# Kernel tuning notes

Hardware: AMD Instinct MI355X
Metric: run time of the kernel (lower is better)

## Reference

```python
import jax, jax.numpy as jnp
import numpy as np

N_E = 16384
E_DIM = 64
BETA = 0.25


def setup_inputs() -> dict:
    key = jax.random.key(0)
    k1, k2 = jax.random.split(key)
    z = jax.random.normal(k1, (8, E_DIM, 32, 32), dtype=jnp.float32)
    # original inits uniform(-1/n_e, 1/n_e); use same scale
    emb_w = jax.random.uniform(k2, (N_E, E_DIM), dtype=jnp.float32,
                               minval=-1.0 / N_E, maxval=1.0 / N_E)
    return {"z": z, "emb_w": emb_w}


def reference(z, emb_w):
    # b c h w -> b h w c
    zp = jnp.transpose(z, (0, 2, 3, 1))              # [B,H,W,C]
    zf = zp.reshape(-1, E_DIM)                       # [N, e_dim]

    # pairwise squared distances: ||z||^2 + ||e||^2 - 2 z e^T
    d = (jnp.sum(zf * zf, axis=1, keepdims=True)
         + jnp.sum(emb_w * emb_w, axis=1)
         - 2.0 * jnp.einsum('nd,kd->nk', zf, emb_w))  # [N, n_e]
    idx = jnp.argmin(d, axis=1)                      # [N] int

    # usage tracking (codebook_usage starts at zeros each fresh module)
    usage = jnp.zeros((N_E,), dtype=jnp.float32).at[idx].max(1.0)
    num_unique = jnp.sum(usage).astype(jnp.int32)
    total_usage = jnp.sum(usage) / N_E

    z_q = emb_w[idx].reshape(zp.shape)               # [B,H,W,C]

    # legacy loss: ||sg(z_q)-z||^2 + beta*||z_q-sg(z)||^2
    loss = (jnp.mean((jax.lax.stop_gradient(z_q) - zp) ** 2)
            + BETA * jnp.mean((z_q - jax.lax.stop_gradient(zp)) ** 2))

    # straight-through estimator
    z_q = zp + jax.lax.stop_gradient(z_q - zp)
    z_q = jnp.transpose(z_q, (0, 3, 1, 2))           # b h w c -> b c h w

    return (z_q, loss, idx, num_unique, usage, total_usage)
```

## Files before the change

### kernel.cpp

```cpp
#include <hip/hip_runtime.h>
#include <math.h>

#define N_ROWS 8192
#define N_E    16384
#define EDIM   64
#define KSPLIT 16
#define KPER   1024
#define CHUNK  64
#define NCH    (KPER/CHUNK)

#define OFF_ZQ    0
#define OFF_LOSS  524288
#define OFF_IDX   524289
#define OFF_NUNIQ 532481
#define OFF_USAGE 532482
#define OFF_TOTAL 548866

typedef __attribute__((ext_vector_type(8)))  short  short8;
typedef __attribute__((ext_vector_type(8)))  ushort ushort8;
typedef __attribute__((ext_vector_type(4)))  float  f32x4;

__device__ ushort g_eh[N_E * EDIM];
__device__ ushort g_zh[N_ROWS * EDIM];
__device__ float  g_zt[N_ROWS * EDIM];

__device__ __forceinline__ ushort bf16hi(float v) {
    unsigned u = __float_as_uint(v);
    return (ushort)((u + 0x7fffu + ((u >> 16) & 1u)) >> 16);
}

__global__ __launch_bounds__(256) void vq_split(
    const float* __restrict__ z, const float* __restrict__ emb,
    float* __restrict__ anorm, float* __restrict__ out,
    float* __restrict__ lossacc, unsigned* __restrict__ done)
{
    __shared__ float lds[64][129];
    int bid = blockIdx.x, t = threadIdx.x;
    if (bid < 1024) {
        int i = bid * 256 + t;
        float4 v = ((const float4*)emb)[i];
        ushort4 h;
        h.x = bf16hi(v.x); h.y = bf16hi(v.y);
        h.z = bf16hi(v.z); h.w = bf16hi(v.w);
        ((ushort4*)g_eh)[i] = h;
    } else if (bid < 1088) {
        int zb = bid - 1024;
        int b = zb >> 3, hw0 = (zb & 7) << 7;
        const float* zp = z + (size_t)b * 65536 + hw0;
        for (int i = 0; i < 32; i++) {
            int j = i * 256 + t;
            int d = j >> 7, hw = j & 127;
            lds[d][hw] = zp[d * 1024 + hw];
        }
        __syncthreads();
        for (int i = 0; i < 4; i++) {
            int task = i * 256 + t;
            int hw = task >> 3, oct = task & 7;
            ushort8 h8; float4 f0, f1;
            float* fp0 = (float*)&f0; float* fp1 = (float*)&f1;
#pragma unroll
            for (int q = 0; q < 8; q++) {
                float v = lds[oct * 8 + q][hw];
                ((ushort*)&h8)[q] = bf16hi(v);
                if (q < 4) fp0[q] = v; else fp1[q - 4] = v;
            }
            size_t ro = (size_t)(b * 1024 + hw0 + hw) * 64 + oct * 8;
            *(ushort8*)(g_zh + ro) = h8;
            *(float4*)(g_zt + ro) = f0;
            *(float4*)(g_zt + ro + 4) = f1;
        }
        if (t < 128) {
            double s = 0.0;
            for (int d = 0; d < 64; d++) {
                float v = lds[d][t];
                s += (double)(v * v);
            }
            anorm[b * 1024 + hw0 + t] = (float)s;
        }
    } else {
        int i = (bid - 1088) * 256 + t;
        out[OFF_USAGE + i] = 0.f;
        if (bid == 1088 && t == 0) { *lossacc = 0.f; *done = 0u; }
    }
}

__global__ __launch_bounds__(256) void vq_mfma(const float* __restrict__ anorm,
                                               unsigned* __restrict__ pcand)
{
    __shared__ __align__(16) ushort ebuf[2][8][CHUNK][8];

    const int t = threadIdx.x;
    const int w = t >> 6, lane = t & 63;
    const int rb = blockIdx.x >> 4, split = blockIdx.x & 15;
    const int n0 = rb * 128;
    const int nw = n0 + w * 32;
    const int kbase = split * KPER;
    const int col = lane & 15, quad = lane >> 4;

    short8 ah[2][2];
#pragma unroll
    for (int rt = 0; rt < 2; rt++)
#pragma unroll
        for (int s = 0; s < 2; s++) {
            size_t off = (size_t)(nw + rt * 16 + col) * 64 + s * 32 + quad * 8;
            ah[rt][s] = *(const short8*)(g_zh + off);
        }

    float av[8];
#pragma unroll
    for (int rt = 0; rt < 2; rt++)
#pragma unroll
        for (int r = 0; r < 4; r++)
            av[rt * 4 + r] = anorm[nw + rt * 16 + quad * 4 + r];

    unsigned p1[8], p2[8];
#pragma unroll
    for (int s = 0; s < 8; s++) { p1[s] = 0xFFFFFFFFu; p2[s] = 0xFFFFFFFFu; }

    auto stage = [&](int dbuf, int code0) {
#pragma unroll
        for (int jj = 0; jj < 2; jj++) {
            int g = w * 2 + jj;
            const ushort* ga = g_eh + (size_t)(code0 + lane) * 64 + g * 8;
            __builtin_amdgcn_global_load_lds(
                (const __attribute__((address_space(1))) void*)ga,
                (__attribute__((address_space(3))) void*)&ebuf[dbuf][g][0][0],
                16, 0, 0);
        }
    };

    const f32x4 Z = {0.f, 0.f, 0.f, 0.f};
    stage(0, kbase);
    for (int ch = 0; ch < NCH; ch++) {
        int cur = ch & 1;
        if (ch + 1 < NCH) {
            stage(cur ^ 1, kbase + (ch + 1) * CHUNK);
            asm volatile("s_waitcnt vmcnt(2)" ::: "memory");
        } else {
            asm volatile("s_waitcnt vmcnt(0)" ::: "memory");
        }
        __builtin_amdgcn_s_barrier();
        asm volatile("" ::: "memory");
#pragma unroll
        for (int ct = 0; ct < 4; ct++) {
            int cn = ct * 16 + col;
            short8 bh0 = *(const short8*)&ebuf[cur][quad][cn][0];
            short8 bh1 = *(const short8*)&ebuf[cur][4 + quad][cn][0];
            f32x4 a0 = __builtin_amdgcn_mfma_f32_16x16x32_bf16(ah[0][0], bh0, Z, 0, 0, 0);
            f32x4 a1 = __builtin_amdgcn_mfma_f32_16x16x32_bf16(ah[1][0], bh0, Z, 0, 0, 0);
            a0 = __builtin_amdgcn_mfma_f32_16x16x32_bf16(ah[0][1], bh1, a0, 0, 0, 0);
            a1 = __builtin_amdgcn_mfma_f32_16x16x32_bf16(ah[1][1], bh1, a1, 0, 0, 0);

            unsigned slot = (unsigned)(ch * 4 + ct);
#pragma unroll
            for (int rt = 0; rt < 2; rt++)
#pragma unroll
                for (int r = 0; r < 4; r++) {
                    int s = rt * 4 + r;
                    float c = rt ? a1[r] : a0[r];
                    float dq = fmaf(-2.0f, c, av[s]);
                    unsigned e = (__float_as_uint(dq) << 6) | slot;
                    unsigned p2n;
                    asm("v_med3_u32 %0, %1, %2, %3"
                        : "=v"(p2n) : "v"(p1[s]), "v"(p2[s]), "v"(e));
                    p2[s] = p2n;
                    p1[s] = (p1[s] < e) ? p1[s] : e;
                }
        }
        __builtin_amdgcn_s_barrier();
        asm volatile("" ::: "memory");
    }

    unsigned* sc = (unsigned*)ebuf;
#pragma unroll
    for (int s = 0; s < 8; s++) {
        int rt = s >> 2, r = s & 3;
        int lr = w * 32 + rt * 16 + quad * 4 + r;
        unsigned av26 = __float_as_uint(av[s]) & 0x03FFFFFFu;
#pragma unroll
        for (int j = 0; j < 2; j++) {
            unsigned p = j ? p2[s] : p1[s];
            unsigned dq26 = p >> 6;
            int diff = ((int)((dq26 - av26) << 6)) >> 6;
            unsigned packed = ((unsigned)(diff + 32768) << 10)
                            | ((p & 63u) << 4) | (unsigned)col;
            sc[lr * 32 + ((col * 2 + j + lr * 2) & 31)] = packed;
        }
    }
    __syncthreads();
    if (t < 128) {
        unsigned b0 = ~0u, b1 = ~0u, b2 = ~0u, b3 = ~0u;
        for (int q = 0; q < 32; q++) {
            unsigned v = sc[t * 32 + ((q + 2 * t) & 31)];
            unsigned m0 = (b0 > v) ? b0 : v;  b0 = (b0 < v) ? b0 : v;
            unsigned m1 = (b1 > m0) ? b1 : m0; b1 = (b1 < m0) ? b1 : m0;
            unsigned m2 = (b2 > m1) ? b2 : m1; b2 = (b2 < m1) ? b2 : m1;
            b3 = (b3 < m2) ? b3 : m2;
        }
        size_t base = (size_t)(n0 + t) * (KSPLIT * 4) + split * 4;
        pcand[base + 0] = b0; pcand[base + 1] = b1;
        pcand[base + 2] = b2; pcand[base + 3] = b3;
    }
}

__device__ __forceinline__ double shfl_xor_d(double p, int m) {
    int2 u = __builtin_bit_cast(int2, p);
    u.x = __shfl_xor(u.x, m);
    u.y = __shfl_xor(u.y, m);
    return __builtin_bit_cast(double, u);
}
__device__ __forceinline__ unsigned long long shfl_xor_u64(unsigned long long p, int m) {
    int2 u = __builtin_bit_cast(int2, p);
    u.x = __shfl_xor(u.x, m);
    u.y = __shfl_xor(u.y, m);
    return __builtin_bit_cast(unsigned long long, u);
}

__global__ __launch_bounds__(256) void vq_refine(
    const float* __restrict__ emb, const float* __restrict__ anorm,
    const unsigned* __restrict__ pcand,
    float* __restrict__ out, int* __restrict__ idxfin)
{
    int t = threadIdx.x;
    int lane = t & 63;
    int n = blockIdx.x * 4 + (t >> 6);
    int li = lane & 15;
    int qd = lane >> 4;

    float4 zf = *(const float4*)(g_zt + (size_t)n * 64 + li * 4);
    double z0 = (double)zf.x, z1 = (double)zf.y;
    double z2 = (double)zf.z, z3 = (double)zf.w;

    float av = anorm[n];
    unsigned av_b = __float_as_uint(av);

    unsigned v = pcand[(size_t)n * 64 + lane];
    unsigned dqb = av_b + (v >> 10) - 32768u;
    float cd = __uint_as_float(dqb);
    int ck = (lane >> 2) * KPER + (int)((v >> 4) & 63u) * 16 + (int)(v & 15u);

    float mn = cd;
#pragma unroll
    for (int s = 1; s < 64; s <<= 1) mn = fminf(mn, __shfl_xor(mn, s));
    float margin = __uint_as_float(av_b & 0xFF800000u) * 0x1p-18f;
    unsigned long long msk = __ballot(cd <= mn + margin);

    unsigned long long bkey = ~0ull;
    while (msk) {
        int ls[4];
#pragma unroll
        for (int j = 0; j < 4; j++) {
            ls[j] = msk ? (__ffsll((unsigned long long)msk) - 1) : -1;
            if (msk) msk &= msk - 1;
        }
        int lsel = ls[qd];
        int lsafe = (lsel >= 0) ? lsel : 0;
        int kq = __shfl(ck, lsafe);
        int k = (lsel >= 0) ? kq : -1;
        double s = 0.0;
        if (k >= 0) {
            float4 ef = *(const float4*)(emb + (size_t)k * EDIM + li * 4);
            s = fma(z3, (double)ef.w,
                fma(z2, (double)ef.z,
                fma(z1, (double)ef.y, z0 * (double)ef.x)));
        }
        s += shfl_xor_d(s, 1);
        s += shfl_xor_d(s, 2);
        s += shfl_xor_d(s, 4);
        s += shfl_xor_d(s, 8);
        if (k >= 0) {
            float c32 = (float)s;
            float dq = av - 2.0f * c32;
            unsigned long long key =
                ((unsigned long long)__float_as_uint(dq) << 32) | (unsigned)k;
            bkey = (key < bkey) ? key : bkey;
        }
    }
#pragma unroll
    for (int m = 1; m < 64; m <<= 1) {
        unsigned long long o = shfl_xor_u64(bkey, m);
        bkey = (o < bkey) ? o : bkey;
    }
    if (lane == 0) {
        int bk = (int)(unsigned)(bkey & 0xffffffffu);
        idxfin[n] = bk;
        out[OFF_IDX + n] = (float)bk;
        out[OFF_USAGE + bk] = 1.0f;
    }
}

__global__ __launch_bounds__(256) void vq_gather(
    const float* __restrict__ z, const float* __restrict__ emb,
    const int* __restrict__ idxfin, float* __restrict__ out,
    float* __restrict__ lossacc, unsigned* __restrict__ done)
{
    __shared__ float buf[32][65];
    __shared__ float red[4];
    __shared__ unsigned lastflag;
    int t = threadIdx.x, w = t >> 6, lane = t & 63;
    int n0 = blockIdx.x * 32;
    int b = n0 >> 10, hw0 = n0 & 1023;
    for (int rr = 0; rr < 8; rr++) {
        int rl = w * 8 + rr;
        int k = idxfin[n0 + rl];
        buf[rl][lane] = emb[(size_t)k * 64 + lane];
    }
    __syncthreads();
    float ls = 0.f;
    int hw_i = t & 31, c0 = t >> 5;
    for (int cc = 0; cc < 8; cc++) {
        int c = c0 * 8 + cc;
        int o = b * 65536 + c * 1024 + hw0 + hw_i;
        float zq = buf[hw_i][c];
        float zv = z[o];
        out[OFF_ZQ + o] = zq;
        float d = zq - zv;
        ls = fmaf(d, d, ls);
    }
#pragma unroll
    for (int s = 1; s < 64; s <<= 1) ls += __shfl_xor(ls, s);
    if (lane == 0) red[w] = ls;
    __syncthreads();
    if (t == 0) {
        atomicAdd(lossacc, red[0] + red[1] + red[2] + red[3]);
        __threadfence();
        unsigned old = atomicAdd(done, 1u);
        lastflag = (old == 255u) ? 1u : 0u;
    }
    __syncthreads();
    if (lastflag) {
        float s = 0.f;
        for (int i = 0; i < 64; i++) s += out[OFF_USAGE + t + i * 256];
#pragma unroll
        for (int sh = 1; sh < 64; sh <<= 1) s += __shfl_xor(s, sh);
        if (lane == 0) red[w] = s;
        __syncthreads();
        if (t == 0) {
            __threadfence();
            float total = atomicAdd(lossacc, 0.0f);
            float cnt = red[0] + red[1] + red[2] + red[3];
            out[OFF_NUNIQ] = cnt;
            out[OFF_TOTAL] = cnt / 16384.0f;
            out[OFF_LOSS]  = total * 1.25f / 524288.0f;
        }
    }
}

extern "C" void kernel_launch(void* const* d_in, const int* in_sizes, int n_in,
                              void* d_out, int out_size, void* d_ws, size_t ws_size,
                              hipStream_t stream)
{
    const float* z   = (const float*)d_in[0];
    const float* emb = (const float*)d_in[1];
    float* out = (float*)d_out;
    char* ws = (char*)d_ws;

    float*    anorm   = (float*)ws;
    unsigned* pcand   = (unsigned*)(ws + 32768);
    int*      idxfin  = (int*)(ws + 32768 + 2097152);
    float*    lossacc = (float*)(ws + 32768 + 2097152 + 32768);
    unsigned* done    = (unsigned*)(ws + 32768 + 2097152 + 32768 + 4);

    vq_split <<<1152, 256, 0, stream>>>(z, emb, anorm, out, lossacc, done);
    vq_mfma  <<<(N_ROWS / 128) * KSPLIT, 256, 0, stream>>>(anorm, pcand);
    vq_refine<<<N_ROWS / 4, 256, 0, stream>>>(emb, anorm, pcand, out, idxfin);
    vq_gather<<<256, 256, 0, stream>>>(z, emb, idxfin, out, lossacc, done);
}
```

Measured before the change: 119.3 us.

## Fuse codebook gather and loss into refine kernel, add deterministic finale reduction

The gather of the chosen codebook rows, the z_q transpose write and the per-row squared-error loss move into the refine kernel, so the separate gather kernel and the idxfin round trip through memory go away. Each refine block writes a partial loss to the workspace. A single-block finale kernel then sums the partials in double precision and counts usage, replacing the atomic and last-block-done scheme. The z_q stores from refine are now only four contiguous floats per channel row, so writes are less coalesced, and the finale still costs a kernel launch.

```diff
diff --git a/kernel.cpp b/kernel.cpp
--- a/kernel.cpp
+++ b/kernel.cpp
@@ -31,8 +31,7 @@
 
 __global__ __launch_bounds__(256) void vq_split(
     const float* __restrict__ z, const float* __restrict__ emb,
-    float* __restrict__ anorm, float* __restrict__ out,
-    float* __restrict__ lossacc, unsigned* __restrict__ done)
+    float* __restrict__ anorm, float* __restrict__ out)
 {
     __shared__ float lds[64][129];
     int bid = blockIdx.x, t = threadIdx.x;
@@ -80,7 +79,6 @@
     } else {
         int i = (bid - 1088) * 256 + t;
         out[OFF_USAGE + i] = 0.f;
-        if (bid == 1088 && t == 0) { *lossacc = 0.f; *done = 0u; }
     }
 }
 
@@ -219,11 +217,14 @@
 __global__ __launch_bounds__(256) void vq_refine(
     const float* __restrict__ emb, const float* __restrict__ anorm,
     const unsigned* __restrict__ pcand,
-    float* __restrict__ out, int* __restrict__ idxfin)
-{
+    float* __restrict__ out, float* __restrict__ lossp)
+{
+    __shared__ float zq_s[4][65];
+    __shared__ float red[4];
     int t = threadIdx.x;
     int lane = t & 63;
-    int n = blockIdx.x * 4 + (t >> 6);
+    int wv = t >> 6;
+    int n = blockIdx.x * 4 + wv;
     int li = lane & 15;
     int qd = lane >> 4;
 
@@ -281,68 +282,52 @@
         unsigned long long o = shfl_xor_u64(bkey, m);
         bkey = (o < bkey) ? o : bkey;
     }
+    int bk = (int)(unsigned)(bkey & 0xffffffffu);
     if (lane == 0) {
-        int bk = (int)(unsigned)(bkey & 0xffffffffu);
-        idxfin[n] = bk;
         out[OFF_IDX + n] = (float)bk;
         out[OFF_USAGE + bk] = 1.0f;
     }
-}
-
-__global__ __launch_bounds__(256) void vq_gather(
-    const float* __restrict__ z, const float* __restrict__ emb,
-    const int* __restrict__ idxfin, float* __restrict__ out,
-    float* __restrict__ lossacc, unsigned* __restrict__ done)
-{
-    __shared__ float buf[32][65];
-    __shared__ float red[4];
-    __shared__ unsigned lastflag;
-    int t = threadIdx.x, w = t >> 6, lane = t & 63;
-    int n0 = blockIdx.x * 32;
-    int b = n0 >> 10, hw0 = n0 & 1023;
-    for (int rr = 0; rr < 8; rr++) {
-        int rl = w * 8 + rr;
-        int k = idxfin[n0 + rl];
-        buf[rl][lane] = emb[(size_t)k * 64 + lane];
-    }
+    float zqv = emb[(size_t)bk * 64 + lane];
+    zq_s[wv][lane] = zqv;
+    float d = zqv - g_zt[(size_t)n * 64 + lane];
+    float ls = d * d;
+#pragma unroll
+    for (int s = 1; s < 64; s <<= 1) ls += __shfl_xor(ls, s);
+    if (lane == 0) red[wv] = ls;
     __syncthreads();
-    float ls = 0.f;
-    int hw_i = t & 31, c0 = t >> 5;
-    for (int cc = 0; cc < 8; cc++) {
-        int c = c0 * 8 + cc;
-        int o = b * 65536 + c * 1024 + hw0 + hw_i;
-        float zq = buf[hw_i][c];
-        float zv = z[o];
-        out[OFF_ZQ + o] = zq;
-        float d = zq - zv;
-        ls = fmaf(d, d, ls);
-    }
-#pragma unroll
-    for (int s = 1; s < 64; s <<= 1) ls += __shfl_xor(ls, s);
-    if (lane == 0) red[w] = ls;
+    {
+        int nb = blockIdx.x * 4;
+        int b = nb >> 10, hw0 = nb & 1023;
+        int c = t >> 2, i = t & 3;
+        out[OFF_ZQ + b * 65536 + c * 1024 + hw0 + i] = zq_s[i][c];
+    }
+    if (t == 0) lossp[blockIdx.x] = red[0] + red[1] + red[2] + red[3];
+}
+
+__global__ __launch_bounds__(256) void vq_finale(
+    const float* __restrict__ lossp, float* __restrict__ out)
+{
+    __shared__ double redd[4];
+    __shared__ float  redf[4];
+    int t = threadIdx.x, lane = t & 63, wv = t >> 6;
+    float s = 0.f;
+    for (int i = 0; i < 64; i++) s += out[OFF_USAGE + t + i * 256];
+#pragma unroll
+    for (int m = 1; m < 64; m <<= 1) s += __shfl_xor(s, m);
+    if (lane == 0) redf[wv] = s;
+    double ds = 0.0;
+    for (int i = 0; i < 8; i++) ds += (double)lossp[t + i * 256];
+    ds += shfl_xor_d(ds, 1);  ds += shfl_xor_d(ds, 2);
+    ds += shfl_xor_d(ds, 4);  ds += shfl_xor_d(ds, 8);
+    ds += shfl_xor_d(ds, 16); ds += shfl_xor_d(ds, 32);
+    if (lane == 0) redd[wv] = ds;
     __syncthreads();
     if (t == 0) {
-        atomicAdd(lossacc, red[0] + red[1] + red[2] + red[3]);
-        __threadfence();
-        unsigned old = atomicAdd(done, 1u);
-        lastflag = (old == 255u) ? 1u : 0u;
-    }
-    __syncthreads();
-    if (lastflag) {
-        float s = 0.f;
-        for (int i = 0; i < 64; i++) s += out[OFF_USAGE + t + i * 256];
-#pragma unroll
-        for (int sh = 1; sh < 64; sh <<= 1) s += __shfl_xor(s, sh);
-        if (lane == 0) red[w] = s;
-        __syncthreads();
-        if (t == 0) {
-            __threadfence();
-            float total = atomicAdd(lossacc, 0.0f);
-            float cnt = red[0] + red[1] + red[2] + red[3];
-            out[OFF_NUNIQ] = cnt;
-            out[OFF_TOTAL] = cnt / 16384.0f;
-            out[OFF_LOSS]  = total * 1.25f / 524288.0f;
-        }
+        float cnt = redf[0] + redf[1] + redf[2] + redf[3];
+        double total = redd[0] + redd[1] + redd[2] + redd[3];
+        out[OFF_NUNIQ] = cnt;
+        out[OFF_TOTAL] = cnt / 16384.0f;
+        out[OFF_LOSS]  = (float)(total * 1.25 / 524288.0);
     }
 }
 
@@ -355,14 +340,12 @@
     float* out = (float*)d_out;
     char* ws = (char*)d_ws;
 
-    float*    anorm   = (float*)ws;
-    unsigned* pcand   = (unsigned*)(ws + 32768);
-    int*      idxfin  = (int*)(ws + 32768 + 2097152);
-    float*    lossacc = (float*)(ws + 32768 + 2097152 + 32768);
-    unsigned* done    = (unsigned*)(ws + 32768 + 2097152 + 32768 + 4);
-
-    vq_split <<<1152, 256, 0, stream>>>(z, emb, anorm, out, lossacc, done);
+    float*    anorm = (float*)ws;
+    unsigned* pcand = (unsigned*)(ws + 32768);
+    float*    lossp = (float*)(ws + 32768 + 2097152);
+
+    vq_split <<<1152, 256, 0, stream>>>(z, emb, anorm, out);
     vq_mfma  <<<(N_ROWS / 128) * KSPLIT, 256, 0, stream>>>(anorm, pcand);
-    vq_refine<<<N_ROWS / 4, 256, 0, stream>>>(emb, anorm, pcand, out, idxfin);
-    vq_gather<<<256, 256, 0, stream>>>(z, emb, idxfin, out, lossacc, done);
-}
+    vq_refine<<<N_ROWS / 4, 256, 0, stream>>>(emb, anorm, pcand, out, lossp);
+    vq_finale<<<1, 256, 0, stream>>>(lossp, out);
+}
```

Result: faster. 112.4 us (-5.8%).
